# Kernel optimization log

Measured on AMD Instinct MI355X. Metric: run time of the kernel, lower is better.

Reference implementation:

```python
import jax, jax.numpy as jnp
import numpy as np
from functools import partial

T, B, N = 64, 128, 2048
REST = 0.0
SG_WIDTH = 0.25  # sigmoid surrogate temperature

# Parameter initialization mirrors the torch module: inverse-sigmoid of the
# gate/param constants so that sigmoid(param) recovers the intended value.
_GATE = {'alpha': 0.8, 'beta': 0.2, 'gamma': 0.8}
_PAR = {'tau': 0.25, 'Vth': 0.5, 'leak': 0.5 / 8, 'reVth': 0.5, 'conduct': 0.5}

def _inv_sig(p):
    return -np.log(1.0 / p - 1.0)

def _gate_init(g):  # matches -log(1/((g-0.5)*0.5+0.5) - 1)
    return _inv_sig((g - 0.5) * 0.5 + 0.5)

@jax.custom_vjp
def spike(v, thr):
    # forward: heaviside(v - thr); thr is [N], v is [B, N]
    return (v > thr).astype(v.dtype)

def _spike_fwd(v, thr):
    return spike(v, thr), (v, thr)

def _spike_bwd(res, g):
    v, thr = res
    s = jax.nn.sigmoid((v - thr) / SG_WIDTH)
    grad_v = g * s * (1.0 - s) / SG_WIDTH
    # torch backward returns -grad_v for the threshold input (broadcast => sum batch)
    return grad_v, -jnp.sum(grad_v, axis=0)

spike.defvjp(_spike_fwd, _spike_bwd)

def setup_inputs() -> dict:
    key = jax.random.key(0)
    ks = jax.random.split(key, 10)
    d = {'tx': jax.random.normal(ks[0], (T, B, N), dtype=jnp.float32)}
    d['alpha'] = jnp.full((N,), _gate_init(_GATE['alpha']), dtype=jnp.float32)
    d['beta'] = jnp.full((N,), _gate_init(_GATE['beta']), dtype=jnp.float32)
    d['gamma'] = jnp.full((N,), _gate_init(_GATE['gamma']), dtype=jnp.float32)
    d['tau'] = jnp.full((N,), _inv_sig(_PAR['tau']), dtype=jnp.float32)
    d['Vth'] = jnp.full((N,), _inv_sig(_PAR['Vth']), dtype=jnp.float32)
    d['leak'] = jnp.full((N,), _inv_sig(_PAR['leak']), dtype=jnp.float32)
    d['reVth'] = jnp.full((N,), _inv_sig(_PAR['reVth']), dtype=jnp.float32)
    d['conduct'] = jnp.full((T, N), _inv_sig(_PAR['conduct']), dtype=jnp.float32)
    return d

def reference(tx, alpha, beta, gamma, tau, Vth, leak, reVth, conduct):
    al = jax.nn.sigmoid(alpha)            # [N]
    be = jax.nn.sigmoid(beta)
    ga = jax.nn.sigmoid(gamma)
    tau_s = jax.nn.sigmoid(tau)
    Vth_s = jax.nn.sigmoid(Vth)
    leak_s = jax.nn.sigmoid(leak)
    reVth_s = jax.nn.sigmoid(reVth)
    cond_s = jax.nn.sigmoid(conduct)      # [T, N]

    decay_v = (1.0 - al * (1.0 - tau_s))  # [N]
    leak_term = (1.0 - al) * leak_s       # [N]
    reset_w = (1.0 - ga) * reVth_s        # [N]

    def step(carry, inp):
        v, y = carry                      # [B, N] each
        x, c = inp                        # x:[B,N], c:[N]
        I = x * (1.0 - be * (1.0 - c))
        v = decay_v * v * (1.0 - ga * y) - leak_term + I - reset_w * y
        y = spike(v, Vth_s)
        return (v, y), y

    v0 = jnp.full_like(tx[0], REST)
    y0 = jnp.zeros_like(tx[0])
    _, ty = jax.lax.scan(step, (v0, y0), (tx, cond_s))
    return ty  # [T, B, N]
```

## Files before the change

### kernel.cpp

```cpp
#include <hip/hip_runtime.h>
#include <math.h>


__device__ __forceinline__ double dsig(double x) {
    return 1.0 / (1.0 + exp(-x));
}

__global__ void glif_pre_kernel(const float* __restrict__ alpha,
                                const float* __restrict__ beta,
                                const float* __restrict__ gamma,
                                const float* __restrict__ tau,
                                const float* __restrict__ Vth,
                                const float* __restrict__ leak,
                                const float* __restrict__ reVth,
                                const float* __restrict__ conduct,
                                double* __restrict__ wsd,
                                int N, int TN) {
    int i = blockIdx.x * blockDim.x + threadIdx.x;
    if (i >= TN) return;
    int n = i % N;
    double be = dsig((double)beta[n]);
    double cs = dsig((double)conduct[i]);
    wsd[5 * N + i] = 1.0 - be * (1.0 - cs);
    if (i < N) {
        double al     = dsig((double)alpha[i]);
        double ga     = dsig((double)gamma[i]);
        double tau_s  = dsig((double)tau[i]);
        double vth_s  = dsig((double)Vth[i]);
        double leak_s = dsig((double)leak[i]);
        double rev_s  = dsig((double)reVth[i]);
        wsd[0 * N + i] = 1.0 - al * (1.0 - tau_s);
        wsd[1 * N + i] = (1.0 - al) * leak_s;
        wsd[2 * N + i] = (1.0 - ga) * rev_s;
        wsd[3 * N + i] = vth_s;
        wsd[4 * N + i] = ga;
    }
}

__global__ __launch_bounds__(256) void glif_main_kernel(
        const float* __restrict__ tx,
        const double* __restrict__ wsd,
        float* __restrict__ out,
        int T, int B, int N) {
    const int half = N >> 1;
    const int idx = blockIdx.x * blockDim.x + threadIdx.x;
    if (idx >= B * half) return;
    const int b = idx / half;
    const int n = (idx - b * half) << 1;

    const double dv0 = wsd[0 * N + n], dv1 = wsd[0 * N + n + 1];
    const double lt0 = wsd[1 * N + n], lt1 = wsd[1 * N + n + 1];
    const double rw0 = wsd[2 * N + n], rw1 = wsd[2 * N + n + 1];
    const double th0 = wsd[3 * N + n], th1 = wsd[3 * N + n + 1];
    const double om_ga0 = 1.0 - wsd[4 * N + n];
    const double om_ga1 = 1.0 - wsd[4 * N + n + 1];
    const double* __restrict__ icp = wsd + 5 * N + n;

    double v0 = 0.0, v1 = 0.0;
    bool y0 = false, y1 = false;

    const size_t bn = (size_t)b * N + n;
    const float* txp = tx + bn;
    float* op = out + bn;
    const size_t strideTx = (size_t)B * N;

#pragma unroll 4
    for (int t = 0; t < T; ++t) {
        const float2 x = *(const float2*)txp;
        const double ic0 = icp[0], ic1 = icp[1];

        const double I0 = (double)x.x * ic0;
        const double m0 = y0 ? om_ga0 : 1.0;
        const double r0 = y0 ? rw0 : 0.0;
        v0 = dv0 * v0 * m0 - lt0 + I0 - r0;
        y0 = v0 > th0;

        const double I1 = (double)x.y * ic1;
        const double m1 = y1 ? om_ga1 : 1.0;
        const double r1 = y1 ? rw1 : 0.0;
        v1 = dv1 * v1 * m1 - lt1 + I1 - r1;
        y1 = v1 > th1;

        float2 o;
        o.x = y0 ? 1.0f : 0.0f;
        o.y = y1 ? 1.0f : 0.0f;
        *(float2*)op = o;

        txp += strideTx;
        op += strideTx;
        icp += N;
    }
}

__global__ __launch_bounds__(256) void glif_main_inline_kernel(
        const float* __restrict__ tx,
        const float* __restrict__ alpha,
        const float* __restrict__ beta,
        const float* __restrict__ gamma,
        const float* __restrict__ tau,
        const float* __restrict__ Vth,
        const float* __restrict__ leak,
        const float* __restrict__ reVth,
        const float* __restrict__ conduct,
        float* __restrict__ out,
        int T, int B, int N) {
    const int half = N >> 1;
    const int idx = blockIdx.x * blockDim.x + threadIdx.x;
    if (idx >= B * half) return;
    const int b = idx / half;
    const int n = (idx - b * half) << 1;

    const double al0 = dsig((double)alpha[n]), al1 = dsig((double)alpha[n + 1]);
    const double ga0 = dsig((double)gamma[n]), ga1 = dsig((double)gamma[n + 1]);
    const double be0 = dsig((double)beta[n]),  be1 = dsig((double)beta[n + 1]);
    const double ts0 = dsig((double)tau[n]),   ts1 = dsig((double)tau[n + 1]);
    const double th0 = dsig((double)Vth[n]),   th1 = dsig((double)Vth[n + 1]);
    const double ls0 = dsig((double)leak[n]),  ls1 = dsig((double)leak[n + 1]);
    const double rs0 = dsig((double)reVth[n]), rs1 = dsig((double)reVth[n + 1]);
    const double dv0 = 1.0 - al0 * (1.0 - ts0), dv1 = 1.0 - al1 * (1.0 - ts1);
    const double lt0 = (1.0 - al0) * ls0,       lt1 = (1.0 - al1) * ls1;
    const double rw0 = (1.0 - ga0) * rs0,       rw1 = (1.0 - ga1) * rs1;
    const double om_ga0 = 1.0 - ga0, om_ga1 = 1.0 - ga1;

    double v0 = 0.0, v1 = 0.0;
    bool y0 = false, y1 = false;

    const size_t bn = (size_t)b * N + n;
    const float* txp = tx + bn;
    float* op = out + bn;
    const float* cp = conduct + n;
    const size_t strideTx = (size_t)B * N;

    for (int t = 0; t < T; ++t) {
        const float2 x = *(const float2*)txp;
        const double ic0 = 1.0 - be0 * (1.0 - dsig((double)cp[0]));
        const double ic1 = 1.0 - be1 * (1.0 - dsig((double)cp[1]));

        const double I0 = (double)x.x * ic0;
        const double m0 = y0 ? om_ga0 : 1.0;
        const double r0 = y0 ? rw0 : 0.0;
        v0 = dv0 * v0 * m0 - lt0 + I0 - r0;
        y0 = v0 > th0;

        const double I1 = (double)x.y * ic1;
        const double m1 = y1 ? om_ga1 : 1.0;
        const double r1 = y1 ? rw1 : 0.0;
        v1 = dv1 * v1 * m1 - lt1 + I1 - r1;
        y1 = v1 > th1;

        float2 o;
        o.x = y0 ? 1.0f : 0.0f;
        o.y = y1 ? 1.0f : 0.0f;
        *(float2*)op = o;

        txp += strideTx;
        op += strideTx;
        cp += N;
    }
}

extern "C" void kernel_launch(void* const* d_in, const int* in_sizes, int n_in,
                              void* d_out, int out_size, void* d_ws, size_t ws_size,
                              hipStream_t stream) {
    const float* tx      = (const float*)d_in[0];
    const float* alpha   = (const float*)d_in[1];
    const float* beta    = (const float*)d_in[2];
    const float* gamma   = (const float*)d_in[3];
    const float* tau     = (const float*)d_in[4];
    const float* Vth     = (const float*)d_in[5];
    const float* leak    = (const float*)d_in[6];
    const float* reVth   = (const float*)d_in[7];
    const float* conduct = (const float*)d_in[8];
    float* out = (float*)d_out;

    const int N  = in_sizes[1];
    const int TN = in_sizes[8];
    const int T  = TN / N;
    const int B  = in_sizes[0] / TN;

    const int total = B * (N >> 1);
    const int mainBlocks = (total + 255) / 256;

    const size_t needed = (size_t)(5 * N + TN) * sizeof(double);
    if (ws_size >= needed) {
        double* wsd = (double*)d_ws;
        const int preBlocks = (TN + 255) / 256;
        glif_pre_kernel<<<preBlocks, 256, 0, stream>>>(
            alpha, beta, gamma, tau, Vth, leak, reVth, conduct, wsd, N, TN);
        glif_main_kernel<<<mainBlocks, 256, 0, stream>>>(
            tx, wsd, out, T, B, N);
    } else {
        glif_main_inline_kernel<<<mainBlocks, 256, 0, stream>>>(
            tx, alpha, beta, gamma, tau, Vth, leak, reVth, conduct,
            out, T, B, N);
    }
}
```

Measured before the change: 138.6 us.

## Process four neurons per thread with prefetching and nontemporal vector loads/stores

The main kernel now handles four adjacent neurons per thread instead of two. It uses 16-byte float4 nontemporal loads of tx and nontemporal stores of output, and loads conduct coefficients as double2 pairs. The next timestep's inputs are prefetched in software so load latency overlaps the serial recurrence. This halves the thread count (128*512 = 65536 threads), which lowers parallelism available to hide latency, and adds a (N&3)==0 requirement on the fast path.

```diff
diff --git a/kernel.cpp b/kernel.cpp
--- a/kernel.cpp
+++ b/kernel.cpp
@@ -1,6 +1,9 @@
 #include <hip/hip_runtime.h>
 #include <math.h>
 
+
+typedef float  fx4 __attribute__((ext_vector_type(4)));
+typedef double dx2 __attribute__((ext_vector_type(2)));
 
 __device__ __forceinline__ double dsig(double x) {
     return 1.0 / (1.0 + exp(-x));
@@ -37,57 +40,68 @@
     }
 }
 
-__global__ __launch_bounds__(256) void glif_main_kernel(
+__global__ __launch_bounds__(256) void glif_main4_kernel(
         const float* __restrict__ tx,
         const double* __restrict__ wsd,
         float* __restrict__ out,
         int T, int B, int N) {
-    const int half = N >> 1;
+    const int quar = N >> 2;
     const int idx = blockIdx.x * blockDim.x + threadIdx.x;
-    if (idx >= B * half) return;
-    const int b = idx / half;
-    const int n = (idx - b * half) << 1;
-
-    const double dv0 = wsd[0 * N + n], dv1 = wsd[0 * N + n + 1];
-    const double lt0 = wsd[1 * N + n], lt1 = wsd[1 * N + n + 1];
-    const double rw0 = wsd[2 * N + n], rw1 = wsd[2 * N + n + 1];
-    const double th0 = wsd[3 * N + n], th1 = wsd[3 * N + n + 1];
-    const double om_ga0 = 1.0 - wsd[4 * N + n];
-    const double om_ga1 = 1.0 - wsd[4 * N + n + 1];
-    const double* __restrict__ icp = wsd + 5 * N + n;
-
-    double v0 = 0.0, v1 = 0.0;
-    bool y0 = false, y1 = false;
+    if (idx >= B * quar) return;
+    const int b = idx / quar;
+    const int n = (idx - b * quar) << 2;
+
+    double dv[4], lt[4], rw[4], th[4], omga[4];
+#pragma unroll
+    for (int j = 0; j < 4; ++j) {
+        dv[j]   = wsd[0 * N + n + j];
+        lt[j]   = wsd[1 * N + n + j];
+        rw[j]   = wsd[2 * N + n + j];
+        th[j]   = wsd[3 * N + n + j];
+        omga[j] = 1.0 - wsd[4 * N + n + j];
+    }
+    const double* icp = wsd + 5 * N + n;
+
+    double v[4] = {0.0, 0.0, 0.0, 0.0};
+    bool y[4] = {false, false, false, false};
 
     const size_t bn = (size_t)b * N + n;
     const float* txp = tx + bn;
     float* op = out + bn;
-    const size_t strideTx = (size_t)B * N;
+    const size_t stride = (size_t)B * N;
+
+    fx4 x = __builtin_nontemporal_load((const fx4*)txp);
+    dx2 icA = *(const dx2*)icp;
+    dx2 icB = *(const dx2*)(icp + 2);
 
 #pragma unroll 4
     for (int t = 0; t < T; ++t) {
-        const float2 x = *(const float2*)txp;
-        const double ic0 = icp[0], ic1 = icp[1];
-
-        const double I0 = (double)x.x * ic0;
-        const double m0 = y0 ? om_ga0 : 1.0;
-        const double r0 = y0 ? rw0 : 0.0;
-        v0 = dv0 * v0 * m0 - lt0 + I0 - r0;
-        y0 = v0 > th0;
-
-        const double I1 = (double)x.y * ic1;
-        const double m1 = y1 ? om_ga1 : 1.0;
-        const double r1 = y1 ? rw1 : 0.0;
-        v1 = dv1 * v1 * m1 - lt1 + I1 - r1;
-        y1 = v1 > th1;
-
-        float2 o;
-        o.x = y0 ? 1.0f : 0.0f;
-        o.y = y1 ? 1.0f : 0.0f;
-        *(float2*)op = o;
-
-        txp += strideTx;
-        op += strideTx;
+        fx4 xn;
+        dx2 icAn, icBn;
+        if (t + 1 < T) {
+            xn   = __builtin_nontemporal_load((const fx4*)(txp + stride));
+            icAn = *(const dx2*)(icp + N);
+            icBn = *(const dx2*)(icp + N + 2);
+        }
+
+        const double xs[4] = {(double)x.x, (double)x.y, (double)x.z, (double)x.w};
+        const double ic[4] = {icA.x, icA.y, icB.x, icB.y};
+
+        fx4 ov;
+#pragma unroll
+        for (int j = 0; j < 4; ++j) {
+            const double I = xs[j] * ic[j];
+            const double m = y[j] ? omga[j] : 1.0;
+            const double r = y[j] ? rw[j] : 0.0;
+            v[j] = dv[j] * v[j] * m - lt[j] + I - r;
+            y[j] = v[j] > th[j];
+            ov[j] = y[j] ? 1.0f : 0.0f;
+        }
+        __builtin_nontemporal_store(ov, (fx4*)op);
+
+        x = xn; icA = icAn; icB = icBn;
+        txp += stride;
+        op += stride;
         icp += N;
     }
 }
@@ -178,19 +192,18 @@
     const int T  = TN / N;
     const int B  = in_sizes[0] / TN;
 
-    const int total = B * (N >> 1);
-    const int mainBlocks = (total + 255) / 256;
-
     const size_t needed = (size_t)(5 * N + TN) * sizeof(double);
-    if (ws_size >= needed) {
+    if (ws_size >= needed && (N & 3) == 0) {
         double* wsd = (double*)d_ws;
         const int preBlocks = (TN + 255) / 256;
         glif_pre_kernel<<<preBlocks, 256, 0, stream>>>(
             alpha, beta, gamma, tau, Vth, leak, reVth, conduct, wsd, N, TN);
-        glif_main_kernel<<<mainBlocks, 256, 0, stream>>>(
+        const int total = B * (N >> 2);
+        glif_main4_kernel<<<(total + 255) / 256, 256, 0, stream>>>(
             tx, wsd, out, T, B, N);
     } else {
-        glif_main_inline_kernel<<<mainBlocks, 256, 0, stream>>>(
+        const int total = B * (N >> 1);
+        glif_main_inline_kernel<<<(total + 255) / 256, 256, 0, stream>>>(
             tx, alpha, beta, gamma, tau, Vth, leak, reVth, conduct,
             out, T, B, N);
     }
```

After: 156.9 us. 1.13x slower.

## Use one neuron per thread with nontemporal loads/stores and next-step prefetch

Applied to the files above, without the earlier changes.

The main kernel now assigns one neuron per thread instead of two, doubling the thread count to B*N for more parallelism. It switches tx loads and output stores to nontemporal builtins so streamed data bypasses cache retention. It also software-prefetches the next timestep's input and coefficient before doing the current step's dependent double-precision recurrence. The trade-off is scalar 4-byte accesses in place of float2 vector accesses.

```diff
diff --git a/kernel.cpp b/kernel.cpp
--- a/kernel.cpp
+++ b/kernel.cpp
@@ -37,57 +37,51 @@
     }
 }
 
-__global__ __launch_bounds__(256) void glif_main_kernel(
+__global__ __launch_bounds__(256) void glif_main1_kernel(
         const float* __restrict__ tx,
         const double* __restrict__ wsd,
         float* __restrict__ out,
         int T, int B, int N) {
-    const int half = N >> 1;
     const int idx = blockIdx.x * blockDim.x + threadIdx.x;
-    if (idx >= B * half) return;
-    const int b = idx / half;
-    const int n = (idx - b * half) << 1;
+    if (idx >= B * N) return;
+    const int n = idx % N;
 
-    const double dv0 = wsd[0 * N + n], dv1 = wsd[0 * N + n + 1];
-    const double lt0 = wsd[1 * N + n], lt1 = wsd[1 * N + n + 1];
-    const double rw0 = wsd[2 * N + n], rw1 = wsd[2 * N + n + 1];
-    const double th0 = wsd[3 * N + n], th1 = wsd[3 * N + n + 1];
-    const double om_ga0 = 1.0 - wsd[4 * N + n];
-    const double om_ga1 = 1.0 - wsd[4 * N + n + 1];
-    const double* __restrict__ icp = wsd + 5 * N + n;
+    const double dv   = wsd[0 * N + n];
+    const double lt   = wsd[1 * N + n];
+    const double rw   = wsd[2 * N + n];
+    const double th   = wsd[3 * N + n];
+    const double omga = 1.0 - wsd[4 * N + n];
+    const double* icp = wsd + 5 * N + n;
 
-    double v0 = 0.0, v1 = 0.0;
-    bool y0 = false, y1 = false;
+    double v = 0.0;
+    bool y = false;
 
-    const size_t bn = (size_t)b * N + n;
-    const float* txp = tx + bn;
-    float* op = out + bn;
-    const size_t strideTx = (size_t)B * N;
+    const float* txp = tx + idx;
+    float* op = out + idx;
+    const size_t stride = (size_t)B * N;
+
+    float x   = __builtin_nontemporal_load(txp);
+    double ic = *icp;
 
 #pragma unroll 4
     for (int t = 0; t < T; ++t) {
-        const float2 x = *(const float2*)txp;
-        const double ic0 = icp[0], ic1 = icp[1];
+        float xn = 0.0f;
+        double icn = 0.0;
+        if (t + 1 < T) {
+            xn  = __builtin_nontemporal_load(txp + stride);
+            icn = icp[N];
+        }
 
-        const double I0 = (double)x.x * ic0;
-        const double m0 = y0 ? om_ga0 : 1.0;
-        const double r0 = y0 ? rw0 : 0.0;
-        v0 = dv0 * v0 * m0 - lt0 + I0 - r0;
-        y0 = v0 > th0;
+        const double I = (double)x * ic;
+        const double m = y ? omga : 1.0;
+        const double r = y ? rw : 0.0;
+        v = dv * v * m - lt + I - r;
+        y = v > th;
+        __builtin_nontemporal_store(y ? 1.0f : 0.0f, op);
 
-        const double I1 = (double)x.y * ic1;
-        const double m1 = y1 ? om_ga1 : 1.0;
-        const double r1 = y1 ? rw1 : 0.0;
-        v1 = dv1 * v1 * m1 - lt1 + I1 - r1;
-        y1 = v1 > th1;
-
-        float2 o;
-        o.x = y0 ? 1.0f : 0.0f;
-        o.y = y1 ? 1.0f : 0.0f;
-        *(float2*)op = o;
-
-        txp += strideTx;
-        op += strideTx;
+        x = xn; ic = icn;
+        txp += stride;
+        op  += stride;
         icp += N;
     }
 }
@@ -178,19 +172,18 @@
     const int T  = TN / N;
     const int B  = in_sizes[0] / TN;
 
-    const int total = B * (N >> 1);
-    const int mainBlocks = (total + 255) / 256;
-
     const size_t needed = (size_t)(5 * N + TN) * sizeof(double);
     if (ws_size >= needed) {
         double* wsd = (double*)d_ws;
         const int preBlocks = (TN + 255) / 256;
         glif_pre_kernel<<<preBlocks, 256, 0, stream>>>(
             alpha, beta, gamma, tau, Vth, leak, reVth, conduct, wsd, N, TN);
-        glif_main_kernel<<<mainBlocks, 256, 0, stream>>>(
+        const int total = B * N;
+        glif_main1_kernel<<<(total + 255) / 256, 256, 0, stream>>>(
             tx, wsd, out, T, B, N);
     } else {
-        glif_main_inline_kernel<<<mainBlocks, 256, 0, stream>>>(
+        const int total = B * (N >> 1);
+        glif_main_inline_kernel<<<(total + 255) / 256, 256, 0, stream>>>(
             tx, alpha, beta, gamma, tau, Vth, leak, reVth, conduct,
             out, T, B, N);
     }
```

Measured after the change: 157.4 us. +13.5%, slower.
